# Performance work log

Measured on AMD Instinct MI355X. Metric: run time of the kernel, lower is better.

Reference implementation:

```python
import jax, jax.numpy as jnp
import numpy as np

B, S, D, H = 4, 2048, 2048, 16
DK = D // H  # 128
EPS = 1e-6


def setup_inputs() -> dict:
    key = jax.random.key(0)
    ks = jax.random.split(key, 8)
    scale = 1.0 / np.sqrt(D)
    return {
        "q": jax.random.normal(ks[0], (B, S, D), jnp.float32),
        "k": jax.random.normal(ks[1], (B, S, D), jnp.float32),
        "v": jax.random.normal(ks[2], (B, S, D), jnp.float32),
        "Wq": jax.random.normal(ks[3], (D, D), jnp.float32) * scale,
        "Wk": jax.random.normal(ks[4], (D, D), jnp.float32) * scale,
        "Wv": jax.random.normal(ks[5], (D, D), jnp.float32) * scale,
        "Wo": jax.random.normal(ks[6], (D, D), jnp.float32) * scale,
        "gamma": jnp.ones((D,), jnp.float32),
        "beta": jnp.zeros((D,), jnp.float32),
    }


def reference(q, k, v, Wq, Wk, Wv, Wo, gamma, beta):
    residual = q
    # projections (Linear with weight (out,in): x @ W^T)
    Q = (q @ Wq.T).reshape(B, S, H, DK)
    K = (k @ Wk.T).reshape(B, S, H, DK)
    V = (v @ Wv.T).reshape(B, S, H, DK)
    # faithful to source: permute(2,0,1,3) then flatten -> head-major (H*B, S, DK)
    Q = jnp.transpose(Q, (2, 0, 1, 3)).reshape(H * B, S, DK)
    K = jnp.transpose(K, (2, 0, 1, 3)).reshape(H * B, S, DK)
    V = jnp.transpose(V, (2, 0, 1, 3)).reshape(H * B, S, DK)
    scores = jnp.einsum("nqd,nkd->nqk", Q, K) / jnp.sqrt(jnp.float32(DK))
    attn = jax.nn.softmax(scores, axis=-1)  # (H*B, S, S)
    context = jnp.einsum("nqk,nkd->nqd", attn, V)
    # faithful to source: view (H*B,S,DK) as (B,H,S,DK) (batch-major reinterpretation)
    context = context.reshape(B, H, S, DK)
    context = jnp.transpose(context, (0, 2, 1, 3)).reshape(B, S, H * DK)
    output = context @ Wo.T  # dropout=0.0 (eval)
    output = output + residual
    mean = jnp.mean(output, axis=-1, keepdims=True)
    var = jnp.mean(jnp.square(output - mean), axis=-1, keepdims=True)
    output = (output - mean) / jnp.sqrt(var + EPS) * gamma + beta
    return output, attn
```

## Files before the change

kernel.cpp:

```cpp
#include <hip/hip_runtime.h>
#include <cstdint>

typedef __attribute__((ext_vector_type(8))) short short8;
typedef __attribute__((ext_vector_type(4))) float f32x4;
typedef __attribute__((ext_vector_type(2))) unsigned u32x2;
typedef unsigned short ushort_t;

constexpr int Bc = 4, Sc = 2048, Dc = 2048, Hc = 16, DKc = 128;
constexpr long NTOK = (long)Bc * Sc;
constexpr long OUT_ELEMS = NTOK * (long)Dc;
constexpr float SCALE = 0.08838834764831843f;

__device__ __forceinline__ ushort_t f2bf(float f) {
  unsigned u = __builtin_bit_cast(unsigned, f);
  u = (u + 0x7FFFu + ((u >> 16) & 1u)) >> 16;
  return (ushort_t)u;
}

__device__ __forceinline__ short8 pack8(const f32x4& a, const f32x4& b) {
  short8 h;
  h[0] = (short)f2bf(a[0]); h[1] = (short)f2bf(a[1]);
  h[2] = (short)f2bf(a[2]); h[3] = (short)f2bf(a[3]);
  h[4] = (short)f2bf(b[0]); h[5] = (short)f2bf(b[1]);
  h[6] = (short)f2bf(b[2]); h[7] = (short)f2bf(b[3]);
  return h;
}

__device__ __forceinline__ void gl2lds16(const ushort_t* g, ushort_t* l) {
  __builtin_amdgcn_global_load_lds(
      (__attribute__((address_space(1))) unsigned int*)(g),
      (__attribute__((address_space(3))) unsigned int*)(l), 16, 0, 0);
}

__device__ __forceinline__ void bar() {
  asm volatile("" ::: "memory");
  __builtin_amdgcn_s_barrier();
  asm volatile("" ::: "memory");
}

template<int MODE>
__global__ __launch_bounds__(512, 2)
void gemm256(const ushort_t* __restrict__ Ap, const ushort_t* __restrict__ Bp,
             void* __restrict__ Cp, const float* __restrict__ residual)
{
  __shared__ __align__(16) ushort_t SM[2][2][2][128 * 64];

  const int tid = threadIdx.x, lane = tid & 63, wave = tid >> 6;
  const int wm = wave >> 2, wn = wave & 3;

  const int lin = blockIdx.y * 8 + blockIdx.x;
  const int swz = (lin & 7) * 32 + (lin >> 3);
  const long n0 = (long)(swz & 7) * 256;
  const long m0 = (long)(swz >> 3) * 256;

  constexpr int NT = 32;

  const ushort_t* Ag = Ap + m0 * (long)Dc;
  const ushort_t* Bg = Bp + n0 * (long)Dc;

  auto stage = [&](const ushort_t* gb, ushort_t* dst, int kt, int ht) {
#pragma unroll
    for (int c = 0; c < 2; ++c) {
      int U = (c * 8 + wave) * 64 + lane;
      int row = U >> 3, p = U & 7, u = p ^ (row & 7);
      gl2lds16(gb + (long)(ht * 128 + row) * Dc + kt * 64 + u * 8,
               dst + (c * 8 + wave) * 512);
    }
  };

  stage(Bg, &SM[1][0][0][0], 0, 0);
  stage(Ag, &SM[0][0][0][0], 0, 0);
  stage(Bg, &SM[1][0][1][0], 0, 1);
  stage(Ag, &SM[0][0][1][0], 0, 1);
  stage(Bg, &SM[1][1][0][0], 1, 0);
  stage(Ag, &SM[0][1][0][0], 1, 0);
  asm volatile("s_waitcnt vmcnt(4)" ::: "memory");
  __builtin_amdgcn_s_barrier();
  asm volatile("" ::: "memory");

  f32x4 acc[8][4] = {};

  for (int kt = 0; kt < NT; ++kt) {
    const int cur = kt & 1;
    const ushort_t* Acur = &SM[0][cur][0][0];
    const ushort_t* Bcur = &SM[1][cur][0][0];
    const int k1 = (kt + 1) & (NT - 1);
    const int k2 = (kt + 2) & (NT - 1);
    short8 af[4][2], bq0[2][2], bq1[2][2];

#pragma unroll
    for (int mf = 0; mf < 4; ++mf)
#pragma unroll
      for (int ks = 0; ks < 2; ++ks) {
        int r = mf * 16 + (lane & 15);
        int u = ks * 4 + (lane >> 4), p = u ^ (r & 7);
        af[mf][ks] = *(const short8*)(Acur + wm * (128 * 64) + r * 64 + p * 8);
      }
#pragma unroll
    for (int nf = 0; nf < 2; ++nf)
#pragma unroll
      for (int ks = 0; ks < 2; ++ks) {
        int r = (wn & 1) * 64 + nf * 16 + (lane & 15);
        int u = ks * 4 + (lane >> 4), p = u ^ (r & 7);
        bq0[nf][ks] = *(const short8*)(Bcur + (wn >> 1) * (128 * 64) + r * 64 + p * 8);
      }
    stage(Bg, &SM[1][cur ^ 1][1][0], k1, 1);
    bar();
    __builtin_amdgcn_s_setprio(1);
#pragma unroll
    for (int mf = 0; mf < 4; ++mf)
#pragma unroll
      for (int nf = 0; nf < 2; ++nf)
#pragma unroll
        for (int ks = 0; ks < 2; ++ks)
          acc[mf][nf] = __builtin_amdgcn_mfma_f32_16x16x32_bf16(af[mf][ks], bq0[nf][ks], acc[mf][nf], 0, 0, 0);
    __builtin_amdgcn_s_setprio(0);
    bar();

#pragma unroll
    for (int nf = 0; nf < 2; ++nf)
#pragma unroll
      for (int ks = 0; ks < 2; ++ks) {
        int r = (wn & 1) * 64 + 32 + nf * 16 + (lane & 15);
        int u = ks * 4 + (lane >> 4), p = u ^ (r & 7);
        bq1[nf][ks] = *(const short8*)(Bcur + (wn >> 1) * (128 * 64) + r * 64 + p * 8);
      }
    stage(Ag, &SM[0][cur ^ 1][1][0], k1, 1);
    bar();
    __builtin_amdgcn_s_setprio(1);
#pragma unroll
    for (int mf = 0; mf < 4; ++mf)
#pragma unroll
      for (int nf = 0; nf < 2; ++nf)
#pragma unroll
        for (int ks = 0; ks < 2; ++ks)
          acc[mf][2 + nf] = __builtin_amdgcn_mfma_f32_16x16x32_bf16(af[mf][ks], bq1[nf][ks], acc[mf][2 + nf], 0, 0, 0);
    __builtin_amdgcn_s_setprio(0);
    bar();

#pragma unroll
    for (int mf = 0; mf < 4; ++mf)
#pragma unroll
      for (int ks = 0; ks < 2; ++ks) {
        int r = 64 + mf * 16 + (lane & 15);
        int u = ks * 4 + (lane >> 4), p = u ^ (r & 7);
        af[mf][ks] = *(const short8*)(Acur + wm * (128 * 64) + r * 64 + p * 8);
      }
    stage(Bg, &SM[1][cur][0][0], k2, 0);
    bar();
    __builtin_amdgcn_s_setprio(1);
#pragma unroll
    for (int mf = 0; mf < 4; ++mf)
#pragma unroll
      for (int nf = 0; nf < 2; ++nf)
#pragma unroll
        for (int ks = 0; ks < 2; ++ks)
          acc[4 + mf][nf] = __builtin_amdgcn_mfma_f32_16x16x32_bf16(af[mf][ks], bq0[nf][ks], acc[4 + mf][nf], 0, 0, 0);
    __builtin_amdgcn_s_setprio(0);
    bar();

    stage(Ag, &SM[0][cur][0][0], k2, 0);
    asm volatile("s_waitcnt vmcnt(4)" ::: "memory");
    bar();
    __builtin_amdgcn_s_setprio(1);
#pragma unroll
    for (int mf = 0; mf < 4; ++mf)
#pragma unroll
      for (int nf = 0; nf < 2; ++nf)
#pragma unroll
        for (int ks = 0; ks < 2; ++ks)
          acc[4 + mf][2 + nf] = __builtin_amdgcn_mfma_f32_16x16x32_bf16(af[mf][ks], bq1[nf][ks], acc[4 + mf][2 + nf], 0, 0, 0);
    __builtin_amdgcn_s_setprio(0);
    bar();
  }

  asm volatile("s_waitcnt vmcnt(0)" ::: "memory");

  if constexpr (MODE == 1) {
    bar();
    char* Tb = (char*)&SM[0][0][0][0];
#pragma unroll
    for (int mq = 0; mq < 8; ++mq) {
#pragma unroll
      for (int nq = 0; nq < 4; ++nq) {
        int rg = wm * 128 + (mq >> 2) * 64 + (mq & 3) * 16 + ((lane >> 4) * 4);
        int cg = wn * 64 + (nq >> 1) * 32 + (nq & 1) * 16 + (lane & 15);
        u32x2 t;
        t[0] = (unsigned)f2bf(acc[mq][nq][0]) | ((unsigned)f2bf(acc[mq][nq][1]) << 16);
        t[1] = (unsigned)f2bf(acc[mq][nq][2]) | ((unsigned)f2bf(acc[mq][nq][3]) << 16);
        int off = cg * 512 + (((rg >> 3) ^ (cg & 31)) * 16) + (rg & 7) * 2;
        *(u32x2*)(Tb + off) = t;
      }
    }
    bar();
    const long bq = m0 >> 11;
    const long s0 = m0 & 2047;
#pragma unroll
    for (int i = 0; i < 16; ++i) {
      int row = i * 16 + (tid >> 5);
      int un  = tid & 31;
      int p = un ^ (row & 31);
      short8 val = *(const short8*)(Tb + row * 512 + p * 16);
      long cgg = n0 + row;
      long vtrow = ((cgg >> 7) * 4 + bq) * 128 + (cgg & 127);
      *(short8*)(&((ushort_t*)Cp)[vtrow * (long)Sc + s0 + un * 8]) = val;
    }
  } else {
#pragma unroll
    for (int mq = 0; mq < 8; ++mq) {
#pragma unroll
      for (int nq = 0; nq < 4; ++nq) {
#pragma unroll
        for (int j = 0; j < 4; ++j) {
          long rg = m0 + wm * 128 + (mq >> 2) * 64 + (mq & 3) * 16 + ((lane >> 4) * 4) + j;
          long cg = n0 + wn * 64 + (nq >> 1) * 32 + (nq & 1) * 16 + (lane & 15);
          float val = acc[mq][nq][j];
          if constexpr (MODE == 0) {
            ((ushort_t*)Cp)[rg * (long)Dc + cg] = f2bf(val);
          } else if constexpr (MODE == 3) {
            ((float*)Cp)[rg * (long)Dc + cg] = val + residual[rg * (long)Dc + cg];
          }
        }
      }
    }
  }
}

__global__ __launch_bounds__(256, 2)
void flash_attn(const ushort_t* __restrict__ Qb, const ushort_t* __restrict__ Kb,
                const ushort_t* __restrict__ VT, float* __restrict__ attn,
                ushort_t* __restrict__ Cb)
{
  __shared__ __align__(16) ushort_t Qs[128 * 128];
  __shared__ __align__(16) ushort_t Ks[64 * 128];
  __shared__ __align__(16) ushort_t Vs[128 * 64];
  __shared__ __align__(16) ushort_t Ps[128 * 64];

  const int tid = threadIdx.x, lane = tid & 63, wave = tid >> 6;
  const int wr = wave >> 1, wc = wave & 1;

  const int bid = blockIdx.x;
  const int xcd = bid & 7, slot = bid >> 3;
  const int n = xcd * 8 + (slot >> 4);
  const long m0 = (long)(slot & 15) * 128;
  const int b = n & 3, h = n >> 2;

  const ushort_t* Qg = Qb + ((long)b * Sc) * Dc + (long)h * DKc;
  const ushort_t* Kg = Kb + ((long)b * Sc) * Dc + (long)h * DKc;
  const ushort_t* Vg = VT + (long)n * DKc * (long)Sc;
  float* Pg = attn + (long)n * Sc * (long)Sc;

#pragma unroll
  for (int c8 = 0; c8 < 8; ++c8) {
    int chunk = c8 * 4 + wave;
    int U = chunk * 64 + lane;
    int row = U >> 4, p = U & 15, u = p ^ (row & 15);
    gl2lds16(Qg + (m0 + row) * (long)Dc + u * 8, &Qs[chunk * 512]);
  }

  auto kaddr = [&](int t, int c4) -> const short8* {
    int chunk = c4 * 4 + wave;
    int U = chunk * 64 + lane;
    int row = U >> 4, p = U & 15, u = p ^ (row & 15);
    return (const short8*)(Kg + ((long)t * 64 + row) * (long)Dc + u * 8);
  };
  auto vaddr = [&](int t, int c4) -> const short8* {
    int chunk = c4 * 4 + wave;
    int U = chunk * 64 + lane;
    int row = U >> 3, p = U & 7, u = p ^ (row & 7);
    return (const short8*)(Vg + (long)row * Sc + (long)t * 64 + u * 8);
  };

  float rs[4][4] = {};

  short8 kr0 = *kaddr(0, 0), kr1 = *kaddr(0, 1), kr2_ = *kaddr(0, 2), kr3 = *kaddr(0, 3);
  for (int t = 0; t < 32; ++t) {
    __syncthreads();
    *(short8*)(&Ks[(0 * 4 + wave) * 512 + lane * 8]) = kr0;
    *(short8*)(&Ks[(1 * 4 + wave) * 512 + lane * 8]) = kr1;
    *(short8*)(&Ks[(2 * 4 + wave) * 512 + lane * 8]) = kr2_;
    *(short8*)(&Ks[(3 * 4 + wave) * 512 + lane * 8]) = kr3;
    {
      int tn = (t + 1) & 31;
      kr0 = *kaddr(tn, 0); kr1 = *kaddr(tn, 1);
      kr2_ = *kaddr(tn, 2); kr3 = *kaddr(tn, 3);
    }
    __syncthreads();
    f32x4 acc[4][2] = {};
#pragma unroll
    for (int kk = 0; kk < 4; ++kk) {
      short8 af[4], bfr[2];
#pragma unroll
      for (int m = 0; m < 4; ++m) {
        int row = wr * 64 + m * 16 + (lane & 15);
        int p = (kk * 4 + (lane >> 4)) ^ (row & 15);
        af[m] = *(const short8*)(&Qs[row * 128 + p * 8]);
      }
#pragma unroll
      for (int nn = 0; nn < 2; ++nn) {
        int row = wc * 32 + nn * 16 + (lane & 15);
        int p = (kk * 4 + (lane >> 4)) ^ (row & 15);
        bfr[nn] = *(const short8*)(&Ks[row * 128 + p * 8]);
      }
#pragma unroll
      for (int m = 0; m < 4; ++m)
#pragma unroll
        for (int nn = 0; nn < 2; ++nn)
          acc[m][nn] = __builtin_amdgcn_mfma_f32_16x16x32_bf16(af[m], bfr[nn], acc[m][nn], 0, 0, 0);
    }
#pragma unroll
    for (int m = 0; m < 4; ++m)
#pragma unroll
      for (int nn = 0; nn < 2; ++nn)
#pragma unroll
        for (int j = 0; j < 4; ++j)
          rs[m][j] += __expf(acc[m][nn][j] * SCALE);
  }

  short8 k0 = *kaddr(0, 0), k1_ = *kaddr(0, 1), k2_ = *kaddr(0, 2), k3 = *kaddr(0, 3);
  short8 v0 = *vaddr(0, 0), v1 = *vaddr(0, 1), v2 = *vaddr(0, 2), v3 = *vaddr(0, 3);

  float* red = (float*)Ps;
#pragma unroll
  for (int m = 0; m < 4; ++m)
#pragma unroll
    for (int j = 0; j < 4; ++j) {
#pragma unroll
      for (int off = 1; off < 16; off <<= 1)
        rs[m][j] += __shfl_xor(rs[m][j], off);
    }
  __syncthreads();
  if ((lane & 15) == 0) {
#pragma unroll
    for (int m = 0; m < 4; ++m)
#pragma unroll
      for (int j = 0; j < 4; ++j)
        red[wc * 128 + wr * 64 + m * 16 + ((lane >> 4) * 4) + j] = rs[m][j];
  }
  __syncthreads();
  float invl[4][4];
#pragma unroll
  for (int m = 0; m < 4; ++m)
#pragma unroll
    for (int j = 0; j < 4; ++j) {
      int row = wr * 64 + m * 16 + ((lane >> 4) * 4) + j;
      invl[m][j] = 1.f / (red[row] + red[128 + row]);
    }

  f32x4 acco[4][4] = {};
  for (int t = 0; t < 32; ++t) {
    __syncthreads();
    *(short8*)(&Ks[(0 * 4 + wave) * 512 + lane * 8]) = k0;
    *(short8*)(&Ks[(1 * 4 + wave) * 512 + lane * 8]) = k1_;
    *(short8*)(&Ks[(2 * 4 + wave) * 512 + lane * 8]) = k2_;
    *(short8*)(&Ks[(3 * 4 + wave) * 512 + lane * 8]) = k3;
    *(short8*)(&Vs[(0 * 4 + wave) * 512 + lane * 8]) = v0;
    *(short8*)(&Vs[(1 * 4 + wave) * 512 + lane * 8]) = v1;
    *(short8*)(&Vs[(2 * 4 + wave) * 512 + lane * 8]) = v2;
    *(short8*)(&Vs[(3 * 4 + wave) * 512 + lane * 8]) = v3;
    {
      int tn = (t + 1) & 31;
      k0 = *kaddr(tn, 0); k1_ = *kaddr(tn, 1); k2_ = *kaddr(tn, 2); k3 = *kaddr(tn, 3);
      v0 = *vaddr(tn, 0); v1 = *vaddr(tn, 1); v2 = *vaddr(tn, 2); v3 = *vaddr(tn, 3);
    }
    __syncthreads();
    f32x4 acc[4][2] = {};
#pragma unroll
    for (int kk = 0; kk < 4; ++kk) {
      short8 af[4], bfr[2];
#pragma unroll
      for (int m = 0; m < 4; ++m) {
        int row = wr * 64 + m * 16 + (lane & 15);
        int p = (kk * 4 + (lane >> 4)) ^ (row & 15);
        af[m] = *(const short8*)(&Qs[row * 128 + p * 8]);
      }
#pragma unroll
      for (int nn = 0; nn < 2; ++nn) {
        int row = wc * 32 + nn * 16 + (lane & 15);
        int p = (kk * 4 + (lane >> 4)) ^ (row & 15);
        bfr[nn] = *(const short8*)(&Ks[row * 128 + p * 8]);
      }
#pragma unroll
      for (int m = 0; m < 4; ++m)
#pragma unroll
        for (int nn = 0; nn < 2; ++nn)
          acc[m][nn] = __builtin_amdgcn_mfma_f32_16x16x32_bf16(af[m], bfr[nn], acc[m][nn], 0, 0, 0);
    }
#pragma unroll
    for (int m = 0; m < 4; ++m) {
#pragma unroll
      for (int nn = 0; nn < 2; ++nn) {
#pragma unroll
        for (int j = 0; j < 4; ++j) {
          float e = __expf(acc[m][nn][j] * SCALE) * invl[m][j];
          int row = wr * 64 + m * 16 + ((lane >> 4) * 4) + j;
          int col = wc * 32 + nn * 16 + (lane & 15);
          Pg[(m0 + row) * (long)Sc + (long)t * 64 + col] = e;
          int pp = (col >> 3) ^ (row & 7);
          Ps[row * 64 + pp * 8 + (col & 7)] = (ushort_t)f2bf(e);
        }
      }
    }
    __syncthreads();
#pragma unroll
    for (int ks = 0; ks < 2; ++ks) {
      short8 pa[4], vb[4];
#pragma unroll
      for (int m = 0; m < 4; ++m) {
        int row = wr * 64 + m * 16 + (lane & 15);
        int p = (ks * 4 + (lane >> 4)) ^ (row & 7);
        pa[m] = *(const short8*)(&Ps[row * 64 + p * 8]);
      }
#pragma unroll
      for (int nn = 0; nn < 4; ++nn) {
        int row = wc * 64 + nn * 16 + (lane & 15);
        int p = (ks * 4 + (lane >> 4)) ^ (row & 7);
        vb[nn] = *(const short8*)(&Vs[row * 64 + p * 8]);
      }
#pragma unroll
      for (int m = 0; m < 4; ++m)
#pragma unroll
        for (int nn = 0; nn < 4; ++nn)
          acco[m][nn] = __builtin_amdgcn_mfma_f32_16x16x32_bf16(pa[m], vb[nn], acco[m][nn], 0, 0, 0);
    }
  }

#pragma unroll
  for (int m = 0; m < 4; ++m) {
#pragma unroll
    for (int nn = 0; nn < 4; ++nn) {
#pragma unroll
      for (int j = 0; j < 4; ++j) {
        int row = wr * 64 + m * 16 + ((lane >> 4) * 4) + j;
        int col = wc * 64 + nn * 16 + (lane & 15);
        Cb[((long)(n >> 4) * Sc + m0 + row) * (long)Dc + (long)(n & 15) * DKc + col] =
            (ushort_t)f2bf(acco[m][nn][j]);
      }
    }
  }
}

__global__ __launch_bounds__(256)
void cast3_bf16(const float* __restrict__ a, const float* __restrict__ b,
                const float* __restrict__ c, ushort_t* __restrict__ oa,
                ushort_t* __restrict__ ob, ushort_t* __restrict__ oc) {
  const float* in = (blockIdx.y == 0) ? a : (blockIdx.y == 1) ? b : c;
  ushort_t* out = (blockIdx.y == 0) ? oa : (blockIdx.y == 1) ? ob : oc;
  long i = ((long)blockIdx.x * 256 + threadIdx.x) * 8;
  f32x4 x = *(const f32x4*)(in + i);
  f32x4 y = *(const f32x4*)(in + i + 4);
  *(short8*)(out + i) = pack8(x, y);
}

__global__ __launch_bounds__(256)
void castW_bf16(const float* __restrict__ w0, const float* __restrict__ w1,
                const float* __restrict__ w2, const float* __restrict__ w3,
                ushort_t* __restrict__ o0, ushort_t* __restrict__ o1,
                ushort_t* __restrict__ o2, ushort_t* __restrict__ o3) {
  const float* in; ushort_t* out;
  switch (blockIdx.y) {
    case 0: in = w0; out = o0; break;
    case 1: in = w1; out = o1; break;
    case 2: in = w2; out = o2; break;
    default: in = w3; out = o3; break;
  }
  long i = ((long)blockIdx.x * 256 + threadIdx.x) * 8;
  f32x4 x = *(const f32x4*)(in + i);
  f32x4 y = *(const f32x4*)(in + i + 4);
  *(short8*)(out + i) = pack8(x, y);
}

__global__ __launch_bounds__(256)
void layernorm_rows(float* __restrict__ out, const float* __restrict__ gamma,
                    const float* __restrict__ beta) {
  const long row = blockIdx.x;
  float* p = out + row * (long)Dc;
  const int tid = threadIdx.x;
  const int lane = tid & 63, wave = tid >> 6;
  f32x4 v0 = *(const f32x4*)(p + tid * 8);
  f32x4 v1 = *(const f32x4*)(p + tid * 8 + 4);
  float s = 0.f, ss = 0.f;
#pragma unroll
  for (int e = 0; e < 4; ++e) { s += v0[e]; ss += v0[e] * v0[e]; }
#pragma unroll
  for (int e = 0; e < 4; ++e) { s += v1[e]; ss += v1[e] * v1[e]; }
  for (int off = 32; off > 0; off >>= 1) { s += __shfl_xor(s, off); ss += __shfl_xor(ss, off); }
  __shared__ float rs_[4], rss_[4];
  if (lane == 0) { rs_[wave] = s; rss_[wave] = ss; }
  __syncthreads();
  s  = rs_[0] + rs_[1] + rs_[2] + rs_[3];
  ss = rss_[0] + rss_[1] + rss_[2] + rss_[3];
  const float mean = s * (1.f / Dc);
  const float var  = ss * (1.f / Dc) - mean * mean;
  const float rstd = rsqrtf(var + 1e-6f);
  f32x4 g0 = *(const f32x4*)(gamma + tid * 8);
  f32x4 g1 = *(const f32x4*)(gamma + tid * 8 + 4);
  f32x4 b0 = *(const f32x4*)(beta + tid * 8);
  f32x4 b1 = *(const f32x4*)(beta + tid * 8 + 4);
#pragma unroll
  for (int e = 0; e < 4; ++e) v0[e] = (v0[e] - mean) * rstd * g0[e] + b0[e];
#pragma unroll
  for (int e = 0; e < 4; ++e) v1[e] = (v1[e] - mean) * rstd * g1[e] + b1[e];
  *(f32x4*)(p + tid * 8) = v0;
  *(f32x4*)(p + tid * 8 + 4) = v1;
}

extern "C" void kernel_launch(void* const* d_in, const int* in_sizes, int n_in,
                              void* d_out, int out_size, void* d_ws, size_t ws_size,
                              hipStream_t stream) {
  (void)in_sizes; (void)n_in; (void)out_size; (void)ws_size;
  const float* q  = (const float*)d_in[0];
  const float* k  = (const float*)d_in[1];
  const float* v  = (const float*)d_in[2];
  const float* Wq = (const float*)d_in[3];
  const float* Wk = (const float*)d_in[4];
  const float* Wv = (const float*)d_in[5];
  const float* Wo = (const float*)d_in[6];
  const float* gamma = (const float*)d_in[7];
  const float* beta  = (const float*)d_in[8];

  float* out  = (float*)d_out;
  float* attn = out + OUT_ELEMS;

  ushort_t* Wqb = (ushort_t*)d_ws;
  ushort_t* Wkb = Wqb + (long)Dc * Dc;
  ushort_t* Wvb = Wkb + (long)Dc * Dc;
  ushort_t* Wob = Wvb + (long)Dc * Dc;
  ushort_t* Qb  = Wob + (long)Dc * Dc;
  ushort_t* Kb  = Qb + OUT_ELEMS;
  ushort_t* VT  = Kb + OUT_ELEMS;
  ushort_t* Cb  = VT + OUT_ELEMS;

  ushort_t* qb = (ushort_t*)attn;
  ushort_t* kb = qb + OUT_ELEMS;
  ushort_t* vb = kb + OUT_ELEMS;

  dim3 blk(256);
  cast3_bf16<<<dim3(OUT_ELEMS / 2048, 3), blk, 0, stream>>>(q, k, v, qb, kb, vb);
  castW_bf16<<<dim3((long)Dc * Dc / 2048, 4), blk, 0, stream>>>(
      Wq, Wk, Wv, Wo, Wqb, Wkb, Wvb, Wob);

  gemm256<0><<<dim3(8, 32), dim3(512), 0, stream>>>(qb, Wqb, Qb, nullptr);
  gemm256<0><<<dim3(8, 32), dim3(512), 0, stream>>>(kb, Wkb, Kb, nullptr);
  gemm256<1><<<dim3(8, 32), dim3(512), 0, stream>>>(vb, Wvb, VT, nullptr);

  flash_attn<<<dim3(1024), blk, 0, stream>>>(Qb, Kb, VT, attn, Cb);

  gemm256<3><<<dim3(8, 32), dim3(512), 0, stream>>>(Cb, Wob, out, q);

  layernorm_rows<<<NTOK, blk, 0, stream>>>(out, gamma, beta);
}
```

Measured before the change: 765.3 us.

## Fuse fp32-to-bf16 input cast into batched QKV projection GEMM

Removes the separate cast kernel for q/k/v. The projection GEMM now loads fp32 activations through registers, converts them to bf16 and writes them to LDS, overlapping with the MFMA work. The three projection GEMMs are merged into one launch using blockIdx.z. The attention-probability writes use nontemporal stores to reduce cache pollution. In exchange, the GEMM reads twice as many A bytes and adds register pressure plus a VALU conversion step inside the main loop.

```diff
diff --git a/kernel.cpp b/kernel.cpp
--- a/kernel.cpp
+++ b/kernel.cpp
@@ -38,12 +38,20 @@
   asm volatile("" ::: "memory");
 }
 
-template<int MODE>
 __global__ __launch_bounds__(512, 2)
-void gemm256(const ushort_t* __restrict__ Ap, const ushort_t* __restrict__ Bp,
-             void* __restrict__ Cp, const float* __restrict__ residual)
+void proj_gemm(const float* __restrict__ qf, const float* __restrict__ kf,
+               const float* __restrict__ vf,
+               const ushort_t* __restrict__ Wqb, const ushort_t* __restrict__ Wkb,
+               const ushort_t* __restrict__ Wvb,
+               ushort_t* __restrict__ Qb, ushort_t* __restrict__ Kb,
+               ushort_t* __restrict__ VTo)
 {
   __shared__ __align__(16) ushort_t SM[2][2][2][128 * 64];
+
+  const int z = blockIdx.z;
+  const float* Afull = (z == 0) ? qf : (z == 1) ? kf : vf;
+  const ushort_t* Bp = (z == 0) ? Wqb : (z == 1) ? Wkb : Wvb;
+  ushort_t* Cp = (z == 0) ? Qb : (z == 1) ? Kb : VTo;
 
   const int tid = threadIdx.x, lane = tid & 63, wave = tid >> 6;
   const int wm = wave >> 2, wn = wave & 3;
@@ -53,6 +61,213 @@
   const long n0 = (long)(swz & 7) * 256;
   const long m0 = (long)(swz >> 3) * 256;
 
+  constexpr int NT = 32;
+
+  const float*    Ag = Afull + m0 * (long)Dc;
+  const ushort_t* Bg = Bp + n0 * (long)Dc;
+
+  auto stageB = [&](ushort_t* dst, int kt, int ht) {
+#pragma unroll
+    for (int c = 0; c < 2; ++c) {
+      int U = (c * 8 + wave) * 64 + lane;
+      int row = U >> 3, p = U & 7, u = p ^ (row & 7);
+      gl2lds16(Bg + (long)(ht * 128 + row) * Dc + kt * 64 + u * 8,
+               dst + (c * 8 + wave) * 512);
+    }
+  };
+  auto loadA = [&](int kt, f32x4 alo[2][2], f32x4 ahi[2][2]) {
+#pragma unroll
+    for (int ht = 0; ht < 2; ++ht)
+#pragma unroll
+      for (int c = 0; c < 2; ++c) {
+        int U = (c * 8 + wave) * 64 + lane;
+        int row = U >> 3, p = U & 7, u = p ^ (row & 7);
+        const float* g = Ag + (long)(ht * 128 + row) * Dc + kt * 64 + u * 8;
+        alo[ht][c] = *(const f32x4*)g;
+        ahi[ht][c] = *(const f32x4*)(g + 4);
+      }
+  };
+  auto writeA = [&](int buf, const f32x4 alo[2][2], const f32x4 ahi[2][2]) {
+#pragma unroll
+    for (int ht = 0; ht < 2; ++ht)
+#pragma unroll
+      for (int c = 0; c < 2; ++c) {
+        int chunk = c * 8 + wave;
+        *(short8*)(&SM[0][buf][ht][chunk * 512 + lane * 8]) =
+            pack8(alo[ht][c], ahi[ht][c]);
+      }
+  };
+
+  stageB(&SM[1][0][0][0], 0, 0);
+  stageB(&SM[1][0][1][0], 0, 1);
+  stageB(&SM[1][1][0][0], 1, 0);
+  {
+    f32x4 alo[2][2], ahi[2][2];
+    loadA(0, alo, ahi);
+    asm volatile("s_waitcnt vmcnt(0)" ::: "memory");
+    writeA(0, alo, ahi);
+    asm volatile("s_waitcnt lgkmcnt(0)" ::: "memory");
+  }
+  __builtin_amdgcn_s_barrier();
+  asm volatile("" ::: "memory");
+
+  f32x4 acc[8][4] = {};
+
+  for (int kt = 0; kt < NT; ++kt) {
+    const int cur = kt & 1;
+    const ushort_t* Acur = &SM[0][cur][0][0];
+    const ushort_t* Bcur = &SM[1][cur][0][0];
+    const int k1 = (kt + 1) & (NT - 1);
+    const int k2 = (kt + 2) & (NT - 1);
+    short8 af[4][2], bq0[2][2], bq1[2][2];
+    f32x4 alo[2][2], ahi[2][2];
+
+#pragma unroll
+    for (int mf = 0; mf < 4; ++mf)
+#pragma unroll
+      for (int ks = 0; ks < 2; ++ks) {
+        int r = mf * 16 + (lane & 15);
+        int u = ks * 4 + (lane >> 4), p = u ^ (r & 7);
+        af[mf][ks] = *(const short8*)(Acur + wm * (128 * 64) + r * 64 + p * 8);
+      }
+#pragma unroll
+    for (int nf = 0; nf < 2; ++nf)
+#pragma unroll
+      for (int ks = 0; ks < 2; ++ks) {
+        int r = (wn & 1) * 64 + nf * 16 + (lane & 15);
+        int u = ks * 4 + (lane >> 4), p = u ^ (r & 7);
+        bq0[nf][ks] = *(const short8*)(Bcur + (wn >> 1) * (128 * 64) + r * 64 + p * 8);
+      }
+    stageB(&SM[1][cur ^ 1][1][0], k1, 1);
+    bar();
+    __builtin_amdgcn_s_setprio(1);
+#pragma unroll
+    for (int mf = 0; mf < 4; ++mf)
+#pragma unroll
+      for (int nf = 0; nf < 2; ++nf)
+#pragma unroll
+        for (int ks = 0; ks < 2; ++ks)
+          acc[mf][nf] = __builtin_amdgcn_mfma_f32_16x16x32_bf16(af[mf][ks], bq0[nf][ks], acc[mf][nf], 0, 0, 0);
+    __builtin_amdgcn_s_setprio(0);
+    bar();
+
+#pragma unroll
+    for (int nf = 0; nf < 2; ++nf)
+#pragma unroll
+      for (int ks = 0; ks < 2; ++ks) {
+        int r = (wn & 1) * 64 + 32 + nf * 16 + (lane & 15);
+        int u = ks * 4 + (lane >> 4), p = u ^ (r & 7);
+        bq1[nf][ks] = *(const short8*)(Bcur + (wn >> 1) * (128 * 64) + r * 64 + p * 8);
+      }
+    loadA(k1, alo, ahi);
+    bar();
+    __builtin_amdgcn_s_setprio(1);
+#pragma unroll
+    for (int mf = 0; mf < 4; ++mf)
+#pragma unroll
+      for (int nf = 0; nf < 2; ++nf)
+#pragma unroll
+        for (int ks = 0; ks < 2; ++ks)
+          acc[mf][2 + nf] = __builtin_amdgcn_mfma_f32_16x16x32_bf16(af[mf][ks], bq1[nf][ks], acc[mf][2 + nf], 0, 0, 0);
+    __builtin_amdgcn_s_setprio(0);
+    bar();
+
+#pragma unroll
+    for (int mf = 0; mf < 4; ++mf)
+#pragma unroll
+      for (int ks = 0; ks < 2; ++ks) {
+        int r = 64 + mf * 16 + (lane & 15);
+        int u = ks * 4 + (lane >> 4), p = u ^ (r & 7);
+        af[mf][ks] = *(const short8*)(Acur + wm * (128 * 64) + r * 64 + p * 8);
+      }
+    stageB(&SM[1][cur][0][0], k2, 0);
+    bar();
+    __builtin_amdgcn_s_setprio(1);
+#pragma unroll
+    for (int mf = 0; mf < 4; ++mf)
+#pragma unroll
+      for (int nf = 0; nf < 2; ++nf)
+#pragma unroll
+        for (int ks = 0; ks < 2; ++ks)
+          acc[4 + mf][nf] = __builtin_amdgcn_mfma_f32_16x16x32_bf16(af[mf][ks], bq0[nf][ks], acc[4 + mf][nf], 0, 0, 0);
+    __builtin_amdgcn_s_setprio(0);
+    bar();
+
+    asm volatile("s_waitcnt vmcnt(2)" ::: "memory");
+    writeA(cur ^ 1, alo, ahi);
+    asm volatile("s_waitcnt lgkmcnt(0)" ::: "memory");
+    bar();
+    __builtin_amdgcn_s_setprio(1);
+#pragma unroll
+    for (int mf = 0; mf < 4; ++mf)
+#pragma unroll
+      for (int nf = 0; nf < 2; ++nf)
+#pragma unroll
+        for (int ks = 0; ks < 2; ++ks)
+          acc[4 + mf][2 + nf] = __builtin_amdgcn_mfma_f32_16x16x32_bf16(af[mf][ks], bq1[nf][ks], acc[4 + mf][2 + nf], 0, 0, 0);
+    __builtin_amdgcn_s_setprio(0);
+    bar();
+  }
+
+  asm volatile("s_waitcnt vmcnt(0)" ::: "memory");
+
+  if (z == 2) {
+    bar();
+    char* Tb = (char*)&SM[0][0][0][0];
+#pragma unroll
+    for (int mq = 0; mq < 8; ++mq) {
+#pragma unroll
+      for (int nq = 0; nq < 4; ++nq) {
+        int rg = wm * 128 + (mq >> 2) * 64 + (mq & 3) * 16 + ((lane >> 4) * 4);
+        int cg = wn * 64 + (nq >> 1) * 32 + (nq & 1) * 16 + (lane & 15);
+        u32x2 t;
+        t[0] = (unsigned)f2bf(acc[mq][nq][0]) | ((unsigned)f2bf(acc[mq][nq][1]) << 16);
+        t[1] = (unsigned)f2bf(acc[mq][nq][2]) | ((unsigned)f2bf(acc[mq][nq][3]) << 16);
+        int off = cg * 512 + (((rg >> 3) ^ (cg & 31)) * 16) + (rg & 7) * 2;
+        *(u32x2*)(Tb + off) = t;
+      }
+    }
+    bar();
+    const long bq = m0 >> 11;
+    const long s0 = m0 & 2047;
+#pragma unroll
+    for (int i = 0; i < 16; ++i) {
+      int row = i * 16 + (tid >> 5);
+      int un  = tid & 31;
+      int p = un ^ (row & 31);
+      short8 val = *(const short8*)(Tb + row * 512 + p * 16);
+      long cgg = n0 + row;
+      long vtrow = ((cgg >> 7) * 4 + bq) * 128 + (cgg & 127);
+      *(short8*)(&Cp[vtrow * (long)Sc + s0 + un * 8]) = val;
+    }
+  } else {
+#pragma unroll
+    for (int mq = 0; mq < 8; ++mq) {
+#pragma unroll
+      for (int nq = 0; nq < 4; ++nq) {
+#pragma unroll
+        for (int j = 0; j < 4; ++j) {
+          long rg = m0 + wm * 128 + (mq >> 2) * 64 + (mq & 3) * 16 + ((lane >> 4) * 4) + j;
+          long cg = n0 + wn * 64 + (nq >> 1) * 32 + (nq & 1) * 16 + (lane & 15);
+          Cp[rg * (long)Dc + cg] = f2bf(acc[mq][nq][j]);
+        }
+      }
+    }
+  }
+}
+
+__global__ __launch_bounds__(512, 2)
+void out_gemm(const ushort_t* __restrict__ Ap, const ushort_t* __restrict__ Bp,
+              float* __restrict__ Cp, const float* __restrict__ residual)
+{
+  __shared__ __align__(16) ushort_t SM[2][2][2][128 * 64];
+
+  const int tid = threadIdx.x, lane = tid & 63, wave = tid >> 6;
+  const int wm = wave >> 2, wn = wave & 3;
+  const int lin = blockIdx.y * 8 + blockIdx.x;
+  const int swz = (lin & 7) * 32 + (lin >> 3);
+  const long n0 = (long)(swz & 7) * 256;
+  const long m0 = (long)(swz >> 3) * 256;
   constexpr int NT = 32;
 
   const ushort_t* Ag = Ap + m0 * (long)Dc;
@@ -176,51 +391,15 @@
 
   asm volatile("s_waitcnt vmcnt(0)" ::: "memory");
 
-  if constexpr (MODE == 1) {
-    bar();
-    char* Tb = (char*)&SM[0][0][0][0];
-#pragma unroll
-    for (int mq = 0; mq < 8; ++mq) {
-#pragma unroll
-      for (int nq = 0; nq < 4; ++nq) {
-        int rg = wm * 128 + (mq >> 2) * 64 + (mq & 3) * 16 + ((lane >> 4) * 4);
-        int cg = wn * 64 + (nq >> 1) * 32 + (nq & 1) * 16 + (lane & 15);
-        u32x2 t;
-        t[0] = (unsigned)f2bf(acc[mq][nq][0]) | ((unsigned)f2bf(acc[mq][nq][1]) << 16);
-        t[1] = (unsigned)f2bf(acc[mq][nq][2]) | ((unsigned)f2bf(acc[mq][nq][3]) << 16);
-        int off = cg * 512 + (((rg >> 3) ^ (cg & 31)) * 16) + (rg & 7) * 2;
-        *(u32x2*)(Tb + off) = t;
-      }
-    }
-    bar();
-    const long bq = m0 >> 11;
-    const long s0 = m0 & 2047;
-#pragma unroll
-    for (int i = 0; i < 16; ++i) {
-      int row = i * 16 + (tid >> 5);
-      int un  = tid & 31;
-      int p = un ^ (row & 31);
-      short8 val = *(const short8*)(Tb + row * 512 + p * 16);
-      long cgg = n0 + row;
-      long vtrow = ((cgg >> 7) * 4 + bq) * 128 + (cgg & 127);
-      *(short8*)(&((ushort_t*)Cp)[vtrow * (long)Sc + s0 + un * 8]) = val;
-    }
-  } else {
-#pragma unroll
-    for (int mq = 0; mq < 8; ++mq) {
-#pragma unroll
-      for (int nq = 0; nq < 4; ++nq) {
-#pragma unroll
-        for (int j = 0; j < 4; ++j) {
-          long rg = m0 + wm * 128 + (mq >> 2) * 64 + (mq & 3) * 16 + ((lane >> 4) * 4) + j;
-          long cg = n0 + wn * 64 + (nq >> 1) * 32 + (nq & 1) * 16 + (lane & 15);
-          float val = acc[mq][nq][j];
-          if constexpr (MODE == 0) {
-            ((ushort_t*)Cp)[rg * (long)Dc + cg] = f2bf(val);
-          } else if constexpr (MODE == 3) {
-            ((float*)Cp)[rg * (long)Dc + cg] = val + residual[rg * (long)Dc + cg];
-          }
-        }
+#pragma unroll
+  for (int mq = 0; mq < 8; ++mq) {
+#pragma unroll
+    for (int nq = 0; nq < 4; ++nq) {
+#pragma unroll
+      for (int j = 0; j < 4; ++j) {
+        long rg = m0 + wm * 128 + (mq >> 2) * 64 + (mq & 3) * 16 + ((lane >> 4) * 4) + j;
+        long cg = n0 + wn * 64 + (nq >> 1) * 32 + (nq & 1) * 16 + (lane & 15);
+        Cp[rg * (long)Dc + cg] = acc[mq][nq][j] + residual[rg * (long)Dc + cg];
       }
     }
   }
@@ -395,7 +574,7 @@
           float e = __expf(acc[m][nn][j] * SCALE) * invl[m][j];
           int row = wr * 64 + m * 16 + ((lane >> 4) * 4) + j;
           int col = wc * 32 + nn * 16 + (lane & 15);
-          Pg[(m0 + row) * (long)Sc + (long)t * 64 + col] = e;
+          __builtin_nontemporal_store(e, &Pg[(m0 + row) * (long)Sc + (long)t * 64 + col]);
           int pp = (col >> 3) ^ (row & 7);
           Ps[row * 64 + pp * 8 + (col & 7)] = (ushort_t)f2bf(e);
         }
@@ -438,18 +617,6 @@
       }
     }
   }
-}
-
-__global__ __launch_bounds__(256)
-void cast3_bf16(const float* __restrict__ a, const float* __restrict__ b,
-                const float* __restrict__ c, ushort_t* __restrict__ oa,
-                ushort_t* __restrict__ ob, ushort_t* __restrict__ oc) {
-  const float* in = (blockIdx.y == 0) ? a : (blockIdx.y == 1) ? b : c;
-  ushort_t* out = (blockIdx.y == 0) ? oa : (blockIdx.y == 1) ? ob : oc;
-  long i = ((long)blockIdx.x * 256 + threadIdx.x) * 8;
-  f32x4 x = *(const f32x4*)(in + i);
-  f32x4 y = *(const f32x4*)(in + i + 4);
-  *(short8*)(out + i) = pack8(x, y);
 }
 
 __global__ __launch_bounds__(256)
@@ -531,22 +698,15 @@
   ushort_t* VT  = Kb + OUT_ELEMS;
   ushort_t* Cb  = VT + OUT_ELEMS;
 
-  ushort_t* qb = (ushort_t*)attn;
-  ushort_t* kb = qb + OUT_ELEMS;
-  ushort_t* vb = kb + OUT_ELEMS;
-
-  dim3 blk(256);
-  cast3_bf16<<<dim3(OUT_ELEMS / 2048, 3), blk, 0, stream>>>(q, k, v, qb, kb, vb);
-  castW_bf16<<<dim3((long)Dc * Dc / 2048, 4), blk, 0, stream>>>(
+  castW_bf16<<<dim3((long)Dc * Dc / 2048, 4), dim3(256), 0, stream>>>(
       Wq, Wk, Wv, Wo, Wqb, Wkb, Wvb, Wob);
 
-  gemm256<0><<<dim3(8, 32), dim3(512), 0, stream>>>(qb, Wqb, Qb, nullptr);
-  gemm256<0><<<dim3(8, 32), dim3(512), 0, stream>>>(kb, Wkb, Kb, nullptr);
-  gemm256<1><<<dim3(8, 32), dim3(512), 0, stream>>>(vb, Wvb, VT, nullptr);
-
-  flash_attn<<<dim3(1024), blk, 0, stream>>>(Qb, Kb, VT, attn, Cb);
-
-  gemm256<3><<<dim3(8, 32), dim3(512), 0, stream>>>(Cb, Wob, out, q);
-
-  layernorm_rows<<<NTOK, blk, 0, stream>>>(out, gamma, beta);
-}
+  proj_gemm<<<dim3(8, 32, 3), dim3(512), 0, stream>>>(
+      q, k, v, Wqb, Wkb, Wvb, Qb, Kb, VT);
+
+  flash_attn<<<dim3(1024), dim3(256), 0, stream>>>(Qb, Kb, VT, attn, Cb);
+
+  out_gemm<<<dim3(8, 32), dim3(512), 0, stream>>>(Cb, Wob, out, q);
+
+  layernorm_rows<<<NTOK, dim3(256), 0, stream>>>(out, gamma, beta);
+}
```

Result: faster. 719.4 us (median of 2 runs) (-6.0%).
